# Kernel optimization log

Measured on AMD Instinct MI355X. Metric: run time of the kernel, lower is better.

Reference implementation:

```python
import jax, jax.numpy as jnp
import numpy as np

TRIANGLE_TABLE = np.array([
    [-1,-1,-1,-1,-1,-1],[1,0,2,-1,-1,-1],[4,0,3,-1,-1,-1],[1,4,2,1,3,4],
    [3,1,5,-1,-1,-1],[2,3,0,2,5,3],[1,4,0,1,5,4],[4,2,5,-1,-1,-1],
    [4,5,2,-1,-1,-1],[4,1,0,4,5,1],[3,2,0,3,5,2],[1,3,5,-1,-1,-1],
    [4,1,2,4,3,1],[3,0,4,-1,-1,-1],[2,0,1,-1,-1,-1],[-1,-1,-1,-1,-1,-1]], dtype=np.int32)
NUM_TRI_TABLE = np.array([0,1,1,2,1,2,2,1,1,2,2,1,2,1,1,0], dtype=np.int32)
BASE_TET_EDGES = np.array([0,1,0,2,0,3,1,2,1,3,2,3], dtype=np.int32)

NV = 200_000
NT = 800_000

def setup_inputs() -> dict:
    key = jax.random.key(0)
    k1, k2, k3 = jax.random.split(key, 3)
    pos_nx3 = jax.random.normal(k1, (NV, 3), dtype=jnp.float32)
    sdf_n = jax.random.normal(k2, (NV,), dtype=jnp.float32)
    tet_fx4 = jax.random.randint(k3, (NT, 4), 0, NV, dtype=jnp.int32)
    return {"pos_nx3": pos_nx3, "sdf_n": sdf_n, "tet_fx4": tet_fx4}

def map_uv(face_gidx, max_idx):
    # Faithful port of DMTet.map_uv: one 2-triangle UV quad per (potential) tet.
    N = int(np.ceil(np.sqrt((max_idx + 1) // 2)))
    lin = jnp.linspace(0.0, 1.0 - 1.0 / N, N, dtype=jnp.float32)
    tex_y, tex_x = jnp.meshgrid(lin, lin, indexing='ij')
    pad = 0.9 / N
    uvs = jnp.stack([tex_x, tex_y, tex_x + pad, tex_y,
                     tex_x + pad, tex_y + pad, tex_x, tex_y + pad], axis=-1).reshape(-1, 2)
    t = face_gidx // 2
    tet_idx = (t // N) * N + (t % N)   # identity for t < N*N, kept faithful
    tri_idx = face_gidx % 2
    uv_idx = jnp.stack([tet_idx * 4, tet_idx * 4 + tri_idx + 1, tet_idx * 4 + tri_idx + 2], axis=-1)
    return uvs, uv_idx.reshape(-1, 3)

def reference(pos_nx3, sdf_n, tet_fx4):
    # NOTE: marching-tets output sizes are data dependent -> eager (non-jit) jax,
    # matching the torch.unique / boolean-mask structure of the original.
    tri_table = jnp.asarray(TRIANGLE_TABLE)
    num_tri_table = jnp.asarray(NUM_TRI_TABLE)
    base_edges = jnp.asarray(BASE_TET_EDGES)

    occ_n = sdf_n > 0                                   # [Nv]
    occ_fx4 = occ_n[tet_fx4]                            # [T,4]
    occ_sum = occ_fx4.sum(-1)
    valid_tets = (occ_sum > 0) & (occ_sum < 4)

    tet_valid = tet_fx4[valid_tets]                     # [Tv,4]
    all_edges = tet_valid[:, base_edges].reshape(-1, 2) # [Tv*6,2]
    all_edges = jnp.sort(all_edges, axis=1)             # == sort_edges
    unique_edges, idx_map = jnp.unique(all_edges, axis=0, return_inverse=True)

    mask_edges = occ_n[unique_edges].sum(-1) == 1       # sign-crossing edges
    mapping = jnp.where(mask_edges, jnp.cumsum(mask_edges) - 1, -1)
    idx_map = mapping[idx_map.reshape(-1)].reshape(-1, 6)
    interp_v = unique_edges[mask_edges]                 # [Ne,2]

    # linear interpolation of crossing point along each edge
    p = pos_nx3[interp_v]                               # [Ne,2,3]
    s = sdf_n[interp_v] * jnp.array([1.0, -1.0], dtype=sdf_n.dtype)  # negate 2nd sdf
    denom = s.sum(1, keepdims=True)                     # [Ne,1]
    w = s[:, ::-1] / denom                              # flip + normalize
    verts = (p * w[:, :, None]).sum(1)                  # [Ne,3]

    v_id = jnp.array([1, 2, 4, 8], dtype=jnp.int32)
    tetindex = (occ_fx4[valid_tets].astype(jnp.int32) * v_id).sum(-1)  # [Tv]
    num_triangles = num_tri_table[tetindex]
    m1 = num_triangles == 1
    m2 = num_triangles == 2
    f1 = jnp.take_along_axis(idx_map[m1], tri_table[tetindex[m1]][:, :3], axis=1).reshape(-1, 3)
    f2 = jnp.take_along_axis(idx_map[m2], tri_table[tetindex[m2]][:, :6], axis=1).reshape(-1, 3)
    faces = jnp.concatenate([f1, f2], axis=0)

    num_tets = tet_fx4.shape[0]
    tet_gidx = jnp.arange(num_tets, dtype=jnp.int32)[valid_tets]
    face_gidx = jnp.concatenate([
        tet_gidx[m1] * 2,
        jnp.stack([tet_gidx[m2] * 2, tet_gidx[m2] * 2 + 1], axis=-1).reshape(-1)], axis=0)

    uvs, uv_idx = map_uv(face_gidx, num_tets * 2)
    return verts, faces, uvs, uv_idx
```

## Files before the change

### kernel.cpp

```cpp
#include <hip/hip_runtime.h>
#include <cstdio>
#include <cstdint>

typedef unsigned long long u64;

static const int kNV = 200000;
static const int kNT = 800000;
static const int kNUV = 895;
#define UVS_ROWS   3204100LL
#define UVS_FLOATS 6408200LL
#define CAP 3300000

#define NH 392
#define TILE_T 2048
#define BINW 256
#define NBIN 782
#define SUBSH 15
#define FINEB 2048

#define FB 256
#define FH 32
#define FW (FB + 2*FH)

__device__ const int c_tri[16][6] = {
    {-1,-1,-1,-1,-1,-1},{1,0,2,-1,-1,-1},{4,0,3,-1,-1,-1},{1,4,2,1,3,4},
    {3,1,5,-1,-1,-1},{2,3,0,2,5,3},{1,4,0,1,5,4},{4,2,5,-1,-1,-1},
    {4,5,2,-1,-1,-1},{4,1,0,4,5,1},{3,2,0,3,5,2},{1,3,5,-1,-1,-1},
    {4,1,2,4,3,1},{3,0,4,-1,-1,-1},{2,0,1,-1,-1,-1},{-1,-1,-1,-1,-1,-1}};
__device__ const int c_ntri[16]   = {0,1,1,2,1,2,2,1,1,2,2,1,2,1,1,0};
__device__ const int c_ncross[16] = {0,3,3,4,3,4,4,3,3,4,4,3,4,3,3,0};
__device__ const int c_edges[12] = {0,1,0,2,0,3,1,2,1,3,2,3};

#define PK(m1,m2,nc) (((u64)(m1) << 44) | ((u64)(m2) << 24) | (u64)(nc))

#define SCAN_B 256
#define SCAN_I 8
#define SCAN_TILE (SCAN_B*SCAN_I)

template<typename T>
__global__ void k_scan_partial(const T* __restrict__ in, T* __restrict__ partials, int n){
  __shared__ T sm[SCAN_B];
  int b = blockIdx.x;
  long long base = (long long)b*SCAN_TILE;
  T sum = 0;
  for (int i = threadIdx.x; i < SCAN_TILE; i += SCAN_B){
    long long idx = base + i;
    if (idx < n) sum += in[idx];
  }
  sm[threadIdx.x] = sum; __syncthreads();
  for (int s = SCAN_B/2; s > 0; s >>= 1){
    if ((int)threadIdx.x < s) sm[threadIdx.x] += sm[threadIdx.x + s];
    __syncthreads();
  }
  if (threadIdx.x == 0) partials[b] = sm[0];
}

template<typename T>
__global__ void k_scan_blocksums(T* __restrict__ partials, int nb, T* __restrict__ total_out){
  __shared__ T sm[SCAN_B];
  T carry = 0;
  for (int base = 0; base < nb; base += SCAN_B){
    int i = base + (int)threadIdx.x;
    T v = (i < nb) ? partials[i] : (T)0;
    sm[threadIdx.x] = v; __syncthreads();
    for (int off = 1; off < SCAN_B; off <<= 1){
      T t = ((int)threadIdx.x >= off) ? sm[threadIdx.x - off] : (T)0;
      __syncthreads();
      sm[threadIdx.x] += t;
      __syncthreads();
    }
    if (i < nb) partials[i] = carry + sm[threadIdx.x] - v;
    T tilesum = sm[SCAN_B-1];
    __syncthreads();
    carry += tilesum;
  }
  if (threadIdx.x == 0 && total_out) *total_out = carry;
}

template<typename T>
__global__ void k_scan_apply(const T* __restrict__ in, T* __restrict__ out,
                             const T* __restrict__ partials, int n){
  __shared__ T sm[SCAN_B];
  int b = blockIdx.x;
  long long base = (long long)b*SCAN_TILE + (long long)threadIdx.x*SCAN_I;
  T v[SCAN_I]; T s = 0;
  #pragma unroll
  for (int k = 0; k < SCAN_I; k++){ long long idx = base + k; v[k] = (idx < n) ? in[idx] : (T)0; s += v[k]; }
  sm[threadIdx.x] = s; __syncthreads();
  for (int off = 1; off < 256; off <<= 1){
    T t = ((int)threadIdx.x >= off) ? sm[threadIdx.x - off] : (T)0;
    __syncthreads();
    sm[threadIdx.x] += t;
    __syncthreads();
  }
  T excl = sm[threadIdx.x] - s + partials[b];
  #pragma unroll
  for (int k = 0; k < SCAN_I; k++){ long long idx = base + k; if (idx < n) out[idx] = excl; excl += v[k]; }
}

template<typename T>
static void run_scan(const T* in, T* out, int n, T* partials, hipStream_t s){
  int nb = (n + SCAN_TILE - 1) / SCAN_TILE;
  k_scan_partial<T><<<nb, SCAN_B, 0, s>>>(in, partials, n);
  k_scan_blocksums<T><<<1, SCAN_B, 0, s>>>(partials, nb, out + n);
  k_scan_apply<T><<<nb, SCAN_B, 0, s>>>(in, out, partials, n);
}


__global__ void k_classify_hist(const int* __restrict__ tet, const float* __restrict__ sdf,
                                int* __restrict__ tetinfo, u64* __restrict__ pk,
                                int* __restrict__ blockHist, u64* __restrict__ pkPart){
  __shared__ int h[NBIN];
  __shared__ u64 red[256];
  int blk = blockIdx.x;
  for (int j = threadIdx.x; j < NBIN; j += 256) h[j] = 0;
  __syncthreads();
  int t0 = blk*TILE_T;
  u64 myPk = 0;
  for (int k = 0; k < TILE_T/256; k++){
    int t = t0 + k*256 + threadIdx.x;
    if (t < kNT){
      int4 v4 = ((const int4*)tet)[t];
      int pat = ((sdf[v4.x] > 0.0f) ? 1 : 0) | ((sdf[v4.y] > 0.0f) ? 2 : 0)
              | ((sdf[v4.z] > 0.0f) ? 4 : 0) | ((sdf[v4.w] > 0.0f) ? 8 : 0);
      tetinfo[t] = pat;
      int nt_ = c_ntri[pat];
      u64 pv = PK(nt_ == 1, nt_ == 2, c_ncross[pat]);
      pk[t] = pv;
      myPk += pv;
      if (pat != 0 && pat != 15){
        int vv[4] = {v4.x, v4.y, v4.z, v4.w};
        #pragma unroll
        for (int e = 0; e < 6; e++){
          int i0 = c_edges[2*e], i1 = c_edges[2*e+1];
          if (((pat >> i0) & 1) != ((pat >> i1) & 1)){
            int a = vv[i0], b = vv[i1]; if (a > b){ int tm = a; a = b; b = tm; }
            atomicAdd(&h[a >> 8], 1);
          }
        }
      }
    }
  }
  red[threadIdx.x] = myPk;
  __syncthreads();
  for (int s = 128; s > 0; s >>= 1){
    if ((int)threadIdx.x < s) red[threadIdx.x] += red[threadIdx.x + s];
    __syncthreads();
  }
  if (threadIdx.x == 0) pkPart[blk] = red[0];
  for (int j = threadIdx.x; j < NBIN; j += 256) blockHist[j*NH + blk] = h[j];
}

__global__ void k_scatter(const int* __restrict__ tet, const int* __restrict__ tetinfo,
                          const u64* __restrict__ psum, const int* __restrict__ bhScan,
                          u64* __restrict__ ebin){
  __shared__ int c[NBIN];
  int blk = blockIdx.x;
  for (int j = threadIdx.x; j < NBIN; j += 256) c[j] = bhScan[j*NH + blk];
  __syncthreads();
  int t0 = blk*TILE_T;
  for (int k = 0; k < TILE_T/256; k++){
    int t = t0 + k*256 + threadIdx.x;
    if (t < kNT){
      int pat = tetinfo[t];
      if (pat != 0 && pat != 15){
        int4 v4 = ((const int4*)tet)[t];
        int vv[4] = {v4.x, v4.y, v4.z, v4.w};
        int seq = (int)(psum[t] & 0xFFFFFF);
        #pragma unroll
        for (int e = 0; e < 6; e++){
          int i0 = c_edges[2*e], i1 = c_edges[2*e+1];
          if (((pat >> i0) & 1) != ((pat >> i1) & 1)){
            int a = vv[i0], b = vv[i1]; if (a > b){ int tm = a; a = b; b = tm; }
            int pos = atomicAdd(&c[a >> 8], 1);
            ebin[pos] = ((u64)(unsigned)a << 40) | ((u64)(unsigned)b << 22) | (unsigned)seq;
            seq++;
          }
        }
      }
    }
  }
}

__global__ void k_fine(const int* __restrict__ bhScan, const u64* __restrict__ ebin,
                       u64* __restrict__ efin){
  __shared__ int h[FINEB];
  __shared__ int ss[256];
  int bin = blockIdx.x;
  int binStart = bhScan[bin*NH];
  int binEnd   = bhScan[(bin+1)*NH];
  int a0 = bin << 8;
  for (int j = threadIdx.x; j < FINEB; j += 256) h[j] = 0;
  __syncthreads();
  for (int i = binStart + threadIdx.x; i < binEnd; i += 256){
    u64 p = ebin[i];
    int a = (int)(p >> 40);
    int bh = (int)((p >> 22) & 0x3FFFF) >> SUBSH;
    atomicAdd(&h[((a - a0) << 3) | bh], 1);
  }
  __syncthreads();
  int tid = threadIdx.x;
  int base8 = tid*8;
  int loc[8]; int s = 0;
  #pragma unroll
  for (int q = 0; q < 8; q++){ loc[q] = h[base8+q]; s += loc[q]; }
  ss[tid] = s; __syncthreads();
  for (int off = 1; off < 256; off <<= 1){
    int v = (tid >= off) ? ss[tid - off] : 0;
    __syncthreads();
    ss[tid] += v;
    __syncthreads();
  }
  int excl = ss[tid] - s;
  #pragma unroll
  for (int q = 0; q < 8; q++){ h[base8+q] = excl; excl += loc[q]; }
  __syncthreads();
  for (int i = binStart + tid; i < binEnd; i += 256){
    u64 p = ebin[i];
    int a = (int)(p >> 40);
    int bh = (int)((p >> 22) & 0x3FFFF) >> SUBSH;
    int pos = binStart + atomicAdd(&h[((a - a0) << 3) | bh], 1);
    efin[pos] = p;
  }
}

__global__ void k_flags(const u64* __restrict__ efin, const int* __restrict__ totp,
                        int* __restrict__ firstI, unsigned* __restrict__ meta){
  __shared__ u64 ld[FW];
  __shared__ unsigned char fl[FW];
  int total = *totp;
  int tid = threadIdx.x;
  long long base = (long long)blockIdx.x * FB;
  long long gi = base + tid;
  if (base >= total){
    if (gi < CAP){ firstI[gi] = 0; meta[gi] = 0; }
    return;
  }
  for (int x = tid; x < FW; x += FB){
    long long g = base - FH + x;
    ld[x] = (g >= 0 && g < total) ? (efin[g] >> 22) : ~0ULL;
  }
  __syncthreads();
  for (int x = tid; x < FW; x += FB){
    u64 key = ld[x];
    u64 grp = key >> SUBSH;
    unsigned char f = 1;
    for (int y = x-1; y >= 0; y--){
      u64 ky = ld[y];
      if ((ky >> SUBSH) != grp) break;
      if (ky == key){ f = 0; break; }
    }
    fl[x] = f;
  }
  __syncthreads();
  if (gi < total){
    int x = FH + tid;
    u64 key = ld[x];
    u64 grp = key >> SUBSH;
    int sx = x; while (sx > 0 && (ld[sx-1] >> SUBSH) == grp) sx--;
    int ex = x+1; while (ex < FW && (ld[ex] >> SUBSH) == grp) ex++;
    int first, rank, off;
    if (sx > 0 && ex < FW){
      first = fl[x];
      int rk = 0;
      for (int y = sx; y < ex; y++) if (fl[y] && ld[y] < key) rk++;
      rank = rk; off = x - sx;
    } else {
      u64 keyg = efin[gi] >> 22;
      u64 grpg = keyg >> SUBSH;
      long long s = gi; while (s > 0 && ((efin[s-1] >> 22) >> SUBSH) == grpg) s--;
      long long e = gi + 1; while (e < total && ((efin[e] >> 22) >> SUBSH) == grpg) e++;
      int f = 1;
      for (long long j = s; j < gi; j++) if ((efin[j] >> 22) == keyg){ f = 0; break; }
      int rk = 0;
      for (long long j = s; j < e; j++){
        u64 kj = efin[j] >> 22;
        if (kj < keyg){
          bool fj = true;
          for (long long l = s; l < j; l++) if ((efin[l] >> 22) == kj){ fj = false; break; }
          if (fj) rk++;
        }
      }
      first = f; rank = rk; off = (int)(gi - s);
    }
    firstI[gi] = first;
    meta[gi] = (unsigned)rank | ((unsigned)off << 12) | ((unsigned)first << 24);
  } else if (gi < CAP){
    firstI[gi] = 0;
    meta[gi] = 0;
  }
}

__global__ void k_emit(const u64* __restrict__ efin, const int* __restrict__ totp,
                       const int* __restrict__ fscan, const unsigned* __restrict__ meta,
                       const float* __restrict__ pos, const float* __restrict__ sdf,
                       float* __restrict__ out, int* __restrict__ rankBySeq){
  int total = *totp;
  int i = blockIdx.x*256 + threadIdx.x;
  if (i >= total) return;
  u64 p = efin[i];
  unsigned m = meta[i];
  int rank = m & 0xFFF, off = (m >> 12) & 0xFFF, first = (m >> 24) & 1;
  int r = fscan[i - off] + rank;
  __builtin_nontemporal_store(r, &rankBySeq[(int)(p & 0x3FFFFF)]);
  if (first){
    int a = (int)(p >> 40);
    int b = (int)((p >> 22) & 0x3FFFF);
    float sa = sdf[a], sb = sdf[b];
    float denom = sa - sb;
    float w0 = (-sb) / denom;
    float w1 = sa / denom;
    out[3LL*r + 0] = pos[3*a+0]*w0 + pos[3*b+0]*w1;
    out[3LL*r + 1] = pos[3*a+1]*w0 + pos[3*b+1]*w1;
    out[3LL*r + 2] = pos[3*a+2]*w0 + pos[3*b+2]*w1;
  }
}

__global__ void k_faces(const int* __restrict__ tetinfo, const u64* __restrict__ psum,
                        const int* __restrict__ fscan, const int* __restrict__ rankBySeq,
                        float* __restrict__ out){
  int t = blockIdx.x*256 + threadIdx.x; if (t >= kNT) return;
  int pat = tetinfo[t];
  int nt_ = c_ntri[pat];
  if (nt_ == 0) return;
  u64 tot = psum[kNT];
  int Nm1 = (int)(tot >> 44), Nm2 = (int)((tot >> 24) & 0xFFFFF);
  int Ne = fscan[CAP];
  long long faces_off = 3LL*Ne;
  long long uvidx_off = faces_off + 3LL*((long long)Nm1 + 2LL*Nm2) + UVS_FLOATS;
  u64 ps = psum[t];
  int m1v = (int)(ps >> 44), m2v = (int)((ps >> 24) & 0xFFFFF);
  int seq = (int)(ps & 0xFFFFFF);
  int er[6];
  int j = 0;
  #pragma unroll
  for (int e = 0; e < 6; e++){
    int i0 = c_edges[2*e], i1 = c_edges[2*e+1];
    if (((pat >> i0) & 1) != ((pat >> i1) & 1)){
      er[e] = rankBySeq[seq + j];
      j++;
    } else er[e] = -1;
  }
  for (int k = 0; k < nt_; k++){
    long long row = (nt_ == 1) ? (long long)m1v : ((long long)Nm1 + 2LL*m2v + k);
    #pragma unroll
    for (int c = 0; c < 3; c++){
      int slot = c_tri[pat][3*k + c];
      out[faces_off + 3*row + c] = (float)er[slot];
    }
    out[uvidx_off + 3*row + 0] = (float)(4*t);
    out[uvidx_off + 3*row + 1] = (float)(4*t + k + 1);
    out[uvidx_off + 3*row + 2] = (float)(4*t + k + 2);
  }
}

__global__ void k_uvs(const u64* __restrict__ psum, const int* __restrict__ fscan,
                      float* __restrict__ out){
  long long r = (long long)blockIdx.x*256 + threadIdx.x;
  if (r >= UVS_ROWS) return;
  u64 tot = psum[kNT];
  int Nm1 = (int)(tot >> 44), Nm2 = (int)((tot >> 24) & 0xFFFFF);
  int Ne = fscan[CAP];
  long long off = 3LL*Ne + 3LL*((long long)Nm1 + 2LL*Nm2);
  int cell = (int)(r >> 2), k = (int)(r & 3);
  int iy = cell / kNUV, ix = cell - iy*kNUV;
  const float delta = (1.0f - 1.0f/895.0f) / 894.0f;
  const float pad = 0.9f / 895.0f;
  float x = (float)ix * delta, y = (float)iy * delta;
  float u = x + ((k == 1 || k == 2) ? pad : 0.0f);
  float v = y + ((k >= 2) ? pad : 0.0f);
  if ((off & 1) == 0){
    float2 uv = make_float2(u, v);
    *reinterpret_cast<float2*>(&out[off + 2*r]) = uv;
  } else {
    out[off + 2*r]     = u;
    out[off + 2*r + 1] = v;
  }
}

static inline int divup(int a, int b){ return (a + b - 1) / b; }

extern "C" void kernel_launch(void* const* d_in, const int* in_sizes, int n_in,
                              void* d_out, int out_size, void* d_ws, size_t ws_size,
                              hipStream_t stream){
  const float* pos = (const float*)d_in[0];
  const float* sdf = (const float*)d_in[1];
  const int*   tet = (const int*)d_in[2];
  float* out = (float*)d_out;

  char* ws = (char*)d_ws;
  size_t off = 0;
  auto alloc = [&](size_t bytes) -> char* {
    char* p = ws + off; off += (bytes + 255) & ~(size_t)255; return p;
  };
  int* tetinfo     = (int*)alloc((size_t)kNT*4);
  u64* pk          = (u64*)alloc((size_t)kNT*8);
  u64* psum        = (u64*)alloc((size_t)(kNT+1)*8);
  int* blockHist   = (int*)alloc((size_t)NBIN*NH*4);
  int* bhScan      = (int*)alloc((size_t)(NBIN*NH+1)*4);
  u64* ebin        = (u64*)alloc((size_t)CAP*8);
  u64* efin        = (u64*)alloc((size_t)CAP*8);
  int* rankBySeq   = (int*)alloc((size_t)CAP*4);
  int* fscan       = (int*)alloc((size_t)(CAP+1)*4);
  u64* pkPart      = (u64*)alloc((size_t)NH*8);
  int* partI       = (int*)alloc(4096*4);
  int* firstI      = (int*)ebin;
  unsigned* meta   = (unsigned*)((char*)ebin + (size_t)CAP*4);
  if (off > ws_size){
    fprintf(stderr, "[dmtet] workspace too small: need %zu have %zu\n", off, ws_size);
    return;
  }

  k_classify_hist<<<NH, 256, 0, stream>>>(tet, sdf, tetinfo, pk, blockHist, pkPart);
  k_scan_blocksums<u64><<<1, SCAN_B, 0, stream>>>(pkPart, NH, psum + kNT);
  k_scan_apply<u64><<<divup(kNT,SCAN_TILE), SCAN_B, 0, stream>>>(pk, psum, pkPart, kNT);
  run_scan<int>(blockHist, bhScan, NBIN*NH, partI, stream);
  k_scatter<<<NH, 256, 0, stream>>>(tet, tetinfo, psum, bhScan, ebin);
  k_fine<<<NBIN, 256, 0, stream>>>(bhScan, ebin, efin);
  k_flags<<<divup(CAP,FB), FB, 0, stream>>>(efin, bhScan + NBIN*NH, firstI, meta);
  run_scan<int>(firstI, fscan, CAP, partI, stream);
  k_emit<<<divup(CAP,256), 256, 0, stream>>>(efin, bhScan + NBIN*NH, fscan, meta,
                                             pos, sdf, out, rankBySeq);
  k_faces<<<divup(kNT,256), 256, 0, stream>>>(tetinfo, psum, fscan, rankBySeq, out);
  k_uvs<<<divup((int)UVS_ROWS,256), 256, 0, stream>>>(psum, fscan, out);
}
```

Baseline: 235.0 us.

## Fuse fine bin sort with dedup flags in shared memory, scan per-bin counts

Merges the fine bin sort and the duplicate-flag kernels into one per-bin kernel. It sorts each bin's edges into shared memory, computes first-occurrence flags and per-bin prefix ranks there, and emits a per-bin unique count. The full-size flag scan over CAP entries is replaced by a small scan over bin counts, which removes a global round trip through efin and two kernels. The cost is large shared-memory use per block, which lowers occupancy, plus a very slow single-thread fallback for bins that overflow the shared-memory capacity.

```diff
diff --git a/kernel.cpp b/kernel.cpp
--- a/kernel.cpp
+++ b/kernel.cpp
@@ -17,10 +17,7 @@
 #define NBIN 782
 #define SUBSH 15
 #define FINEB 2048
-
-#define FB 256
-#define FH 32
-#define FW (FB + 2*FH)
+#define MAXBIN 6912
 
 __device__ const int c_tri[16][6] = {
     {-1,-1,-1,-1,-1,-1},{1,0,2,-1,-1,-1},{4,0,3,-1,-1,-1},{1,4,2,1,3,4},
@@ -182,117 +179,148 @@
   }
 }
 
-__global__ void k_fine(const int* __restrict__ bhScan, const u64* __restrict__ ebin,
-                       u64* __restrict__ efin){
+__global__ void k_fineflags(const int* __restrict__ bhScan, const u64* __restrict__ ebin,
+                            u64* __restrict__ efin, unsigned* __restrict__ meta,
+                            int* __restrict__ binFirstCnt){
+  __shared__ u64 ld[MAXBIN];
+  __shared__ unsigned short fp[MAXBIN];
+  __shared__ unsigned char fl[MAXBIN];
   __shared__ int h[FINEB];
   __shared__ int ss[256];
-  int bin = blockIdx.x;
+  __shared__ int totf;
+  int bin = blockIdx.x, tid = threadIdx.x;
   int binStart = bhScan[bin*NH];
   int binEnd   = bhScan[(bin+1)*NH];
+  int n = binEnd - binStart;
   int a0 = bin << 8;
-  for (int j = threadIdx.x; j < FINEB; j += 256) h[j] = 0;
+  for (int j = tid; j < FINEB; j += 256) h[j] = 0;
   __syncthreads();
-  for (int i = binStart + threadIdx.x; i < binEnd; i += 256){
-    u64 p = ebin[i];
-    int a = (int)(p >> 40);
-    int bh = (int)((p >> 22) & 0x3FFFF) >> SUBSH;
-    atomicAdd(&h[((a - a0) << 3) | bh], 1);
-  }
-  __syncthreads();
-  int tid = threadIdx.x;
-  int base8 = tid*8;
-  int loc[8]; int s = 0;
-  #pragma unroll
-  for (int q = 0; q < 8; q++){ loc[q] = h[base8+q]; s += loc[q]; }
-  ss[tid] = s; __syncthreads();
-  for (int off = 1; off < 256; off <<= 1){
-    int v = (tid >= off) ? ss[tid - off] : 0;
-    __syncthreads();
-    ss[tid] += v;
-    __syncthreads();
-  }
-  int excl = ss[tid] - s;
-  #pragma unroll
-  for (int q = 0; q < 8; q++){ h[base8+q] = excl; excl += loc[q]; }
-  __syncthreads();
-  for (int i = binStart + tid; i < binEnd; i += 256){
-    u64 p = ebin[i];
-    int a = (int)(p >> 40);
-    int bh = (int)((p >> 22) & 0x3FFFF) >> SUBSH;
-    int pos = binStart + atomicAdd(&h[((a - a0) << 3) | bh], 1);
-    efin[pos] = p;
-  }
-}
-
-__global__ void k_flags(const u64* __restrict__ efin, const int* __restrict__ totp,
-                        int* __restrict__ firstI, unsigned* __restrict__ meta){
-  __shared__ u64 ld[FW];
-  __shared__ unsigned char fl[FW];
-  int total = *totp;
-  int tid = threadIdx.x;
-  long long base = (long long)blockIdx.x * FB;
-  long long gi = base + tid;
-  if (base >= total){
-    if (gi < CAP){ firstI[gi] = 0; meta[gi] = 0; }
-    return;
-  }
-  for (int x = tid; x < FW; x += FB){
-    long long g = base - FH + x;
-    ld[x] = (g >= 0 && g < total) ? (efin[g] >> 22) : ~0ULL;
-  }
-  __syncthreads();
-  for (int x = tid; x < FW; x += FB){
-    u64 key = ld[x];
-    u64 grp = key >> SUBSH;
-    unsigned char f = 1;
-    for (int y = x-1; y >= 0; y--){
-      u64 ky = ld[y];
-      if ((ky >> SUBSH) != grp) break;
-      if (ky == key){ f = 0; break; }
-    }
-    fl[x] = f;
-  }
-  __syncthreads();
-  if (gi < total){
-    int x = FH + tid;
-    u64 key = ld[x];
-    u64 grp = key >> SUBSH;
-    int sx = x; while (sx > 0 && (ld[sx-1] >> SUBSH) == grp) sx--;
-    int ex = x+1; while (ex < FW && (ld[ex] >> SUBSH) == grp) ex++;
-    int first, rank, off;
-    if (sx > 0 && ex < FW){
-      first = fl[x];
+  if (n <= MAXBIN){
+    for (int i = tid; i < n; i += 256){
+      u64 p = ebin[binStart + i];
+      int key = (((int)(p >> 40) - a0) << 3) | ((int)((p >> 22) & 0x3FFFF) >> SUBSH);
+      atomicAdd(&h[key], 1);
+    }
+    __syncthreads();
+    int base8 = tid*8; int loc[8]; int s = 0;
+    #pragma unroll
+    for (int q = 0; q < 8; q++){ loc[q] = h[base8+q]; s += loc[q]; }
+    ss[tid] = s; __syncthreads();
+    for (int off = 1; off < 256; off <<= 1){
+      int v = (tid >= off) ? ss[tid-off] : 0;
+      __syncthreads(); ss[tid] += v; __syncthreads();
+    }
+    int excl = ss[tid] - s;
+    #pragma unroll
+    for (int q = 0; q < 8; q++){ h[base8+q] = excl; excl += loc[q]; }
+    __syncthreads();
+    for (int i = tid; i < n; i += 256){
+      u64 p = ebin[binStart + i];
+      int key = (((int)(p >> 40) - a0) << 3) | ((int)((p >> 22) & 0x3FFFF) >> SUBSH);
+      ld[atomicAdd(&h[key], 1)] = p;
+    }
+    __syncthreads();
+    for (int x = tid; x < n; x += 256){
+      u64 key = ld[x] >> 22; u64 grp = key >> SUBSH;
+      unsigned char f = 1;
+      for (int y = x-1; y >= 0; y--){
+        u64 ky = ld[y] >> 22;
+        if ((ky >> SUBSH) != grp) break;
+        if (ky == key){ f = 0; break; }
+      }
+      fl[x] = f;
+    }
+    __syncthreads();
+    const int C = MAXBIN/256;
+    int cbase = tid*C;
+    int cs = 0;
+    #pragma unroll
+    for (int q = 0; q < C; q++){ int idx = cbase+q; cs += (idx < n) ? fl[idx] : 0; }
+    ss[tid] = cs; __syncthreads();
+    for (int off = 1; off < 256; off <<= 1){
+      int v = (tid >= off) ? ss[tid-off] : 0;
+      __syncthreads(); ss[tid] += v; __syncthreads();
+    }
+    int ex2 = ss[tid] - cs;
+    #pragma unroll
+    for (int q = 0; q < C; q++){
+      int idx = cbase+q;
+      if (idx < n){ fp[idx] = (unsigned short)ex2; ex2 += fl[idx]; }
+    }
+    if (tid == 255) totf = ss[255];
+    __syncthreads();
+    for (int x = tid; x < n; x += 256){
+      u64 p = ld[x];
+      u64 key = p >> 22; u64 grp = key >> SUBSH;
+      int sx = x; while (sx > 0 && ((ld[sx-1] >> 22) >> SUBSH) == grp) sx--;
+      int ex = x+1; while (ex < n && ((ld[ex] >> 22) >> SUBSH) == grp) ex++;
       int rk = 0;
-      for (int y = sx; y < ex; y++) if (fl[y] && ld[y] < key) rk++;
-      rank = rk; off = x - sx;
-    } else {
-      u64 keyg = efin[gi] >> 22;
-      u64 grpg = keyg >> SUBSH;
-      long long s = gi; while (s > 0 && ((efin[s-1] >> 22) >> SUBSH) == grpg) s--;
-      long long e = gi + 1; while (e < total && ((efin[e] >> 22) >> SUBSH) == grpg) e++;
-      int f = 1;
-      for (long long j = s; j < gi; j++) if ((efin[j] >> 22) == keyg){ f = 0; break; }
-      int rk = 0;
-      for (long long j = s; j < e; j++){
-        u64 kj = efin[j] >> 22;
-        if (kj < keyg){
-          bool fj = true;
-          for (long long l = s; l < j; l++) if ((efin[l] >> 22) == kj){ fj = false; break; }
-          if (fj) rk++;
+      for (int y = sx; y < ex; y++){ if (fl[y] && (ld[y] >> 22) < key) rk++; }
+      int rp = (int)fp[sx] + rk;
+      efin[binStart + x] = p;
+      meta[binStart + x] = ((unsigned)bin << 22) | ((unsigned)rp << 1) | (unsigned)fl[x];
+    }
+    if (tid == 0) binFirstCnt[bin] = totf;
+  } else {
+    for (int i = binStart + tid; i < binEnd; i += 256){
+      u64 p = ebin[i];
+      int key = (((int)(p >> 40) - a0) << 3) | ((int)((p >> 22) & 0x3FFFF) >> SUBSH);
+      atomicAdd(&h[key], 1);
+    }
+    __syncthreads();
+    int base8 = tid*8; int loc[8]; int s = 0;
+    #pragma unroll
+    for (int q = 0; q < 8; q++){ loc[q] = h[base8+q]; s += loc[q]; }
+    ss[tid] = s; __syncthreads();
+    for (int off = 1; off < 256; off <<= 1){
+      int v = (tid >= off) ? ss[tid-off] : 0;
+      __syncthreads(); ss[tid] += v; __syncthreads();
+    }
+    int excl = ss[tid] - s;
+    #pragma unroll
+    for (int q = 0; q < 8; q++){ h[base8+q] = excl; excl += loc[q]; }
+    __syncthreads();
+    for (int i = binStart + tid; i < binEnd; i += 256){
+      u64 p = ebin[i];
+      int key = (((int)(p >> 40) - a0) << 3) | ((int)((p >> 22) & 0x3FFFF) >> SUBSH);
+      efin[binStart + atomicAdd(&h[key], 1)] = p;
+    }
+    __syncthreads();
+    if (tid == 0){
+      int fcnt = 0;
+      for (int x = 0; x < n; x++){
+        u64 key = efin[binStart+x] >> 22; u64 grp = key >> SUBSH;
+        int sx = x; while (sx > 0 && ((efin[binStart+sx-1] >> 22) >> SUBSH) == grp) sx--;
+        int f = 1;
+        for (int y = sx; y < x; y++) if ((efin[binStart+y] >> 22) == key){ f = 0; break; }
+        int fb = 0;
+        for (int y = 0; y < sx; y++){
+          u64 ky = efin[binStart+y] >> 22; u64 gy = ky >> SUBSH;
+          int sy = y; while (sy > 0 && ((efin[binStart+sy-1] >> 22) >> SUBSH) == gy) sy--;
+          int fy = 1;
+          for (int z = sy; z < y; z++) if ((efin[binStart+z] >> 22) == ky){ fy = 0; break; }
+          fb += fy;
         }
+        int ex = x+1; while (ex < n && ((efin[binStart+ex] >> 22) >> SUBSH) == grp) ex++;
+        int rk = 0;
+        for (int y = sx; y < ex; y++){
+          u64 ky = efin[binStart+y] >> 22;
+          if (ky < key){
+            int fy = 1;
+            for (int z = sx; z < y; z++) if ((efin[binStart+z] >> 22) == ky){ fy = 0; break; }
+            if (fy) rk++;
+          }
+        }
+        if (f) fcnt++;
+        meta[binStart+x] = ((unsigned)bin << 22) | ((unsigned)(fb+rk) << 1) | (unsigned)f;
       }
-      first = f; rank = rk; off = (int)(gi - s);
-    }
-    firstI[gi] = first;
-    meta[gi] = (unsigned)rank | ((unsigned)off << 12) | ((unsigned)first << 24);
-  } else if (gi < CAP){
-    firstI[gi] = 0;
-    meta[gi] = 0;
+      binFirstCnt[bin] = fcnt;
+    }
   }
 }
 
 __global__ void k_emit(const u64* __restrict__ efin, const int* __restrict__ totp,
-                       const int* __restrict__ fscan, const unsigned* __restrict__ meta,
+                       const int* __restrict__ binPref, const unsigned* __restrict__ meta,
                        const float* __restrict__ pos, const float* __restrict__ sdf,
                        float* __restrict__ out, int* __restrict__ rankBySeq){
   int total = *totp;
@@ -300,9 +328,11 @@
   if (i >= total) return;
   u64 p = efin[i];
   unsigned m = meta[i];
-  int rank = m & 0xFFF, off = (m >> 12) & 0xFFF, first = (m >> 24) & 1;
-  int r = fscan[i - off] + rank;
-  __builtin_nontemporal_store(r, &rankBySeq[(int)(p & 0x3FFFFF)]);
+  int first = m & 1;
+  int rp = (m >> 1) & 0x1FFFFF;
+  int bin = m >> 22;
+  int r = binPref[bin] + rp;
+  rankBySeq[(int)(p & 0x3FFFFF)] = r;
   if (first){
     int a = (int)(p >> 40);
     int b = (int)((p >> 22) & 0x3FFFF);
@@ -317,7 +347,7 @@
 }
 
 __global__ void k_faces(const int* __restrict__ tetinfo, const u64* __restrict__ psum,
-                        const int* __restrict__ fscan, const int* __restrict__ rankBySeq,
+                        const int* __restrict__ Nep, const int* __restrict__ rankBySeq,
                         float* __restrict__ out){
   int t = blockIdx.x*256 + threadIdx.x; if (t >= kNT) return;
   int pat = tetinfo[t];
@@ -325,7 +355,7 @@
   if (nt_ == 0) return;
   u64 tot = psum[kNT];
   int Nm1 = (int)(tot >> 44), Nm2 = (int)((tot >> 24) & 0xFFFFF);
-  int Ne = fscan[CAP];
+  int Ne = *Nep;
   long long faces_off = 3LL*Ne;
   long long uvidx_off = faces_off + 3LL*((long long)Nm1 + 2LL*Nm2) + UVS_FLOATS;
   u64 ps = psum[t];
@@ -354,13 +384,13 @@
   }
 }
 
-__global__ void k_uvs(const u64* __restrict__ psum, const int* __restrict__ fscan,
+__global__ void k_uvs(const u64* __restrict__ psum, const int* __restrict__ Nep,
                       float* __restrict__ out){
   long long r = (long long)blockIdx.x*256 + threadIdx.x;
   if (r >= UVS_ROWS) return;
   u64 tot = psum[kNT];
   int Nm1 = (int)(tot >> 44), Nm2 = (int)((tot >> 24) & 0xFFFFF);
-  int Ne = fscan[CAP];
+  int Ne = *Nep;
   long long off = 3LL*Ne + 3LL*((long long)Nm1 + 2LL*Nm2);
   int cell = (int)(r >> 2), k = (int)(r & 3);
   int iy = cell / kNUV, ix = cell - iy*kNUV;
@@ -400,12 +430,11 @@
   int* bhScan      = (int*)alloc((size_t)(NBIN*NH+1)*4);
   u64* ebin        = (u64*)alloc((size_t)CAP*8);
   u64* efin        = (u64*)alloc((size_t)CAP*8);
+  unsigned* meta   = (unsigned*)alloc((size_t)CAP*4);
   int* rankBySeq   = (int*)alloc((size_t)CAP*4);
-  int* fscan       = (int*)alloc((size_t)(CAP+1)*4);
+  int* binFirstCnt = (int*)alloc((size_t)(NBIN+1)*4);
   u64* pkPart      = (u64*)alloc((size_t)NH*8);
   int* partI       = (int*)alloc(4096*4);
-  int* firstI      = (int*)ebin;
-  unsigned* meta   = (unsigned*)((char*)ebin + (size_t)CAP*4);
   if (off > ws_size){
     fprintf(stderr, "[dmtet] workspace too small: need %zu have %zu\n", off, ws_size);
     return;
@@ -416,11 +445,10 @@
   k_scan_apply<u64><<<divup(kNT,SCAN_TILE), SCAN_B, 0, stream>>>(pk, psum, pkPart, kNT);
   run_scan<int>(blockHist, bhScan, NBIN*NH, partI, stream);
   k_scatter<<<NH, 256, 0, stream>>>(tet, tetinfo, psum, bhScan, ebin);
-  k_fine<<<NBIN, 256, 0, stream>>>(bhScan, ebin, efin);
-  k_flags<<<divup(CAP,FB), FB, 0, stream>>>(efin, bhScan + NBIN*NH, firstI, meta);
-  run_scan<int>(firstI, fscan, CAP, partI, stream);
-  k_emit<<<divup(CAP,256), 256, 0, stream>>>(efin, bhScan + NBIN*NH, fscan, meta,
+  k_fineflags<<<NBIN, 256, 0, stream>>>(bhScan, ebin, efin, meta, binFirstCnt);
+  k_scan_blocksums<int><<<1, SCAN_B, 0, stream>>>(binFirstCnt, NBIN, binFirstCnt + NBIN);
+  k_emit<<<divup(CAP,256), 256, 0, stream>>>(efin, bhScan + NBIN*NH, binFirstCnt, meta,
                                              pos, sdf, out, rankBySeq);
-  k_faces<<<divup(kNT,256), 256, 0, stream>>>(tetinfo, psum, fscan, rankBySeq, out);
-  k_uvs<<<divup((int)UVS_ROWS,256), 256, 0, stream>>>(psum, fscan, out);
-}
+  k_faces<<<divup(kNT,256), 256, 0, stream>>>(tetinfo, psum, binFirstCnt + NBIN, rankBySeq, out);
+  k_uvs<<<divup((int)UVS_ROWS,256), 256, 0, stream>>>(psum, binFirstCnt + NBIN, out);
+}
```

After: 314.7 us. 33.9% more time.
